# Kernel tuning notes

Hardware: AMD Instinct MI355X
Metric: run time of the kernel (lower is better)

Reference implementation:

```python
import jax, jax.numpy as jnp
import numpy as np

D_HIDDEN = 1024
D_MODEL = 1024
R_MIN, R_MAX = 0.0, 1.0
MAX_PHASE = 6.28
SEQ_LEN = 16384


def setup_inputs() -> dict:
    key = jax.random.key(0)
    k_in, k_th, k_nu, k_bre, k_bim, k_cre, k_cim, k_d = jax.random.split(key, 8)
    inputs = jax.random.normal(k_in, (SEQ_LEN, D_MODEL), dtype=jnp.float32)
    # theta_log ~ log(max_phase * U)
    u_th = jax.random.uniform(k_th, (D_HIDDEN,), dtype=jnp.float32)
    theta_log = jnp.log(MAX_PHASE * u_th)
    # nu_log ~ log(-0.5 * log(U*(r_max^2 - r_min^2) + r_min^2))
    u_nu = jax.random.uniform(k_nu, (D_HIDDEN,), dtype=jnp.float32)
    nu_log = jnp.log(-0.5 * jnp.log(u_nu * (R_MAX**2 - R_MIN**2) + R_MIN**2))
    # gamma_log = log(sqrt(1 - |lambda|^2))
    diag_lambda = jnp.exp(-jnp.exp(nu_log) + 1j * jnp.exp(theta_log))
    gamma_log = jnp.log(jnp.sqrt(1.0 - jnp.abs(diag_lambda) ** 2))
    norm_b = jnp.sqrt(2.0 * D_MODEL)
    norm_c = jnp.sqrt(1.0 * D_HIDDEN)
    B_re = jax.random.normal(k_bre, (D_HIDDEN, D_MODEL), dtype=jnp.float32) / norm_b
    B_im = jax.random.normal(k_bim, (D_HIDDEN, D_MODEL), dtype=jnp.float32) / norm_b
    C_re = jax.random.normal(k_cre, (D_MODEL, D_HIDDEN), dtype=jnp.float32) / norm_c
    C_im = jax.random.normal(k_cim, (D_MODEL, D_HIDDEN), dtype=jnp.float32) / norm_c
    Dp = jax.random.normal(k_d, (D_MODEL,), dtype=jnp.float32)
    return {"inputs": inputs, "nu_log": nu_log, "theta_log": theta_log,
            "gamma_log": gamma_log, "B_re": B_re, "B_im": B_im,
            "C_re": C_re, "C_im": C_im, "Dp": Dp}


def _binop(q_i, q_j):
    # elementwise associative op for diagonal linear recurrence
    A_i, b_i = q_i
    A_j, b_j = q_j
    return (A_j * A_i, A_j * b_i + b_j)


def reference(inputs, nu_log, theta_log, gamma_log, B_re, B_im, C_re, C_im, Dp):
    # diag_lambda: [H] complex64
    diag_lambda = jnp.exp(-jnp.exp(nu_log) + 1j * jnp.exp(theta_log))
    B_norm = (B_re + 1j * B_im) * jnp.exp(gamma_log)[:, None]  # [H, D]
    C = C_re + 1j * C_im                                        # [D, H]
    L = inputs.shape[0]
    # Bu_t = B_norm @ x_t  -> [L, H] complex
    Bu = inputs.astype(B_norm.dtype) @ B_norm.T
    Lambda = jnp.broadcast_to(diag_lambda[None, :], (L, diag_lambda.shape[0]))
    # parallel scan of h_t = lambda * h_{t-1} + Bu_t (initial state = 0)
    _, hidden = jax.lax.associative_scan(_binop, (Lambda, Bu))  # [L, H]
    # y_t = Re[C h_t] + D * x_t
    outputs = jnp.real(hidden @ C.T) + Dp * inputs              # [L, D]
    return (hidden[-1:], outputs)
```

## Files before the change

kernel.cpp:

```cpp
#include <hip/hip_runtime.h>
#include <stdint.h>
#include <stddef.h>

typedef __bf16 bf16;
typedef __attribute__((ext_vector_type(8))) __bf16 bf16x8;
typedef __attribute__((ext_vector_type(4))) __bf16 bf16x4;
typedef __attribute__((ext_vector_type(2))) __bf16 bf16x2;
typedef __attribute__((ext_vector_type(4))) float f32x4;
typedef __attribute__((ext_vector_type(2))) float f32x2;

#define L_SEQ 16384
#define DH    1024
#define DM    1024
#define NH2   2048
#define NC    256
#define LC    (L_SEQ / NC)

__device__ __forceinline__ void async_copy16(const void* g, void* l) {
  __builtin_amdgcn_global_load_lds((const __attribute__((address_space(1))) void*)g,
                                   (__attribute__((address_space(3))) void*)l,
                                   16, 0, 0);
}

__device__ __forceinline__ float bf_lo(uint32_t w) {
  uint32_t u = w << 16; float f; __builtin_memcpy(&f, &u, 4); return f;
}
__device__ __forceinline__ float bf_hi(uint32_t w) {
  uint32_t u = w & 0xffff0000u; float f; __builtin_memcpy(&f, &u, 4); return f;
}

#define NB_CAST 8192
#define NB_W    1024
__global__ void k_prep_all(const float* __restrict__ x, bf16* __restrict__ xb,
                           const float* __restrict__ B_re, const float* __restrict__ B_im,
                           const float* __restrict__ gamma_log, bf16* __restrict__ Wcat,
                           const float* __restrict__ C_re, const float* __restrict__ C_im,
                           bf16* __restrict__ Ccat,
                           const float* __restrict__ nu_log,
                           const float* __restrict__ theta_log,
                           float* __restrict__ lam_re, float* __restrict__ lam_im,
                           float* __restrict__ lamC_re, float* __restrict__ lamC_im) {
  const int b = blockIdx.x;
  if (b < NB_CAST) {
    int i = (b * 256 + (int)threadIdx.x) * 8;
    const float4 a0 = *(const float4*)(x + i);
    const float4 a1 = *(const float4*)(x + i + 4);
    bf16x8 v;
    v[0] = (bf16)a0.x; v[1] = (bf16)a0.y; v[2] = (bf16)a0.z; v[3] = (bf16)a0.w;
    v[4] = (bf16)a1.x; v[5] = (bf16)a1.y; v[6] = (bf16)a1.z; v[7] = (bf16)a1.w;
    *(bf16x8*)(xb + i) = v;
  } else if (b < NB_CAST + NB_W) {
    int idx = ((b - NB_CAST) * 256 + (int)threadIdx.x) * 4;
    int h = idx / DM;
    int d = idx - h * DM;
    float g = expf(gamma_log[h]);
    float4 re = *(const float4*)(B_re + idx);
    float4 im = *(const float4*)(B_im + idx);
    bf16x4 vr, vi;
    vr[0] = (bf16)(re.x * g); vr[1] = (bf16)(re.y * g);
    vr[2] = (bf16)(re.z * g); vr[3] = (bf16)(re.w * g);
    vi[0] = (bf16)(im.x * g); vi[1] = (bf16)(im.y * g);
    vi[2] = (bf16)(im.z * g); vi[3] = (bf16)(im.w * g);
    *(bf16x4*)(Wcat + (size_t)(2 * h) * DM + d)     = vr;
    *(bf16x4*)(Wcat + (size_t)(2 * h + 1) * DM + d) = vi;
  } else if (b < NB_CAST + 2 * NB_W) {
    int idx = ((b - NB_CAST - NB_W) * 256 + (int)threadIdx.x) * 4;
    int d = idx / DH;
    int k = idx - d * DH;
    float4 re = *(const float4*)(C_re + idx);
    float4 im = *(const float4*)(C_im + idx);
    bf16x8 v;
    v[0] = (bf16)re.x; v[1] = (bf16)(-im.x);
    v[2] = (bf16)re.y; v[3] = (bf16)(-im.y);
    v[4] = (bf16)re.z; v[5] = (bf16)(-im.z);
    v[6] = (bf16)re.w; v[7] = (bf16)(-im.w);
    *(bf16x8*)(Ccat + (size_t)d * NH2 + 2 * k) = v;
  } else {
    int h = (b - NB_CAST - 2 * NB_W) * 256 + (int)threadIdx.x;
    if (h < DH) {
      float nu  = expf(nu_log[h]);
      float th  = expf(theta_log[h]);
      float mag = expf(-nu);
      float lr = mag * cosf(th);
      float li = mag * sinf(th);
      lam_re[h] = lr; lam_im[h] = li;
      float ar = lr, ai = li;
#pragma unroll
      for (int i = 0; i < 6; ++i) {
        float nr = ar * ar - ai * ai;
        float ni = 2.f * ar * ai;
        ar = nr; ai = ni;
      }
      lamC_re[h] = ar; lamC_im[h] = ai;
    }
  }
}

template <int MODE>
__global__ __launch_bounds__(256, 3)
void k_gemm(const bf16* __restrict__ A, const bf16* __restrict__ B,
            void* __restrict__ Cout, const float* __restrict__ x,
            const float* __restrict__ dp,
            const float* __restrict__ lam_re, const float* __restrict__ lam_im,
            float* __restrict__ chunk_end, int K, int N) {
  __shared__ char smem[32768];
  bf16* As = (bf16*)smem;
  bf16* Bs = (bf16*)(smem + 16384);
  const int tid  = threadIdx.x;
  const int lane = tid & 63;
  const int wave = tid >> 6;
  const int wm = wave >> 1, wn = wave & 1;
  const int quad = lane >> 4;
  const int l16  = lane & 15;

  const int lin = blockIdx.y * gridDim.x + blockIdx.x;
  const int nY  = gridDim.y;
  const int per = 8 * nY;
  const int sg  = lin / per;
  const int r   = lin - sg * per;
  const int bx  = sg * 8 + (r & 7);
  const int by  = r >> 3;
  const int m0 = bx * 128;
  const int n0 = by * 128;

  f32x4 acc[4][4];
#pragma unroll
  for (int i = 0; i < 4; ++i)
#pragma unroll
    for (int j = 0; j < 4; ++j)
      acc[i][j] = f32x4{0.f, 0.f, 0.f, 0.f};

  for (int k0 = 0; k0 < K; k0 += 64) {
    __syncthreads();
#pragma unroll
    for (int q = 0; q < 4; ++q) {
      const int c = q * 256 + tid;
      const int row = c >> 3, slot = c & 7;
      const int part = slot ^ (row & 7);
      async_copy16(A + (size_t)(m0 + row) * K + k0 + part * 8, (char*)As + c * 16);
      async_copy16(B + (size_t)(n0 + row) * K + k0 + part * 8, (char*)Bs + c * 16);
    }
    __syncthreads();
#pragma unroll
    for (int kk = 0; kk < 64; kk += 32) {
      const int pbase = (kk >> 3);
      bf16x8 fa[4], fb[4];
#pragma unroll
      for (int i = 0; i < 4; ++i) {
        const int ra = wm * 64 + i * 16 + l16;
        const int rb = wn * 64 + i * 16 + l16;
        const int sa = (pbase + quad) ^ (ra & 7);
        const int sb = (pbase + quad) ^ (rb & 7);
        fa[i] = *(const bf16x8*)(As + ra * 64 + sa * 8);
        fb[i] = *(const bf16x8*)(Bs + rb * 64 + sb * 8);
      }
#pragma unroll
      for (int i = 0; i < 4; ++i)
#pragma unroll
        for (int j = 0; j < 4; ++j)
          acc[i][j] = __builtin_amdgcn_mfma_f32_16x16x32_bf16(fa[i], fb[j], acc[i][j], 0, 0, 0);
    }
  }

  if (MODE == 0) {
    __syncthreads();
    bf16* T = (bf16*)smem;
#pragma unroll
    for (int i = 0; i < 4; ++i)
#pragma unroll
      for (int j = 0; j < 4; ++j) {
        const int col = wn * 64 + j * 16 + l16;
        const int grp = col >> 3, cin = col & 7;
#pragma unroll
        for (int p = 0; p < 4; ++p) {
          const int row = wm * 64 + i * 16 + quad * 4 + p;
          T[row * 128 + ((grp ^ (row & 7)) << 3) + cin] = (bf16)acc[i][j][p];
        }
      }
    __syncthreads();
    bf16* out = (bf16*)Cout;
    {
      const int row = tid >> 1, half = tid & 1;
#pragma unroll
      for (int o = 0; o < 8; ++o) {
        const int grp = half * 8 + o;
        bf16x8 v = *(const bf16x8*)(T + row * 128 + ((grp ^ (row & 7)) << 3));
        *(bf16x8*)(out + (size_t)(m0 + row) * N + n0 + grp * 8) = v;
      }
    }
    if (tid < 128) {
      const int ck = tid >> 6;
      const int ch = tid & 63;
      const int gch = (n0 >> 1) + ch;
      const float lr = lam_re[gch], li = lam_im[gch];
      float hr = 0.f, hi = 0.f;
      const int waddr0 = (((ch >> 2) ) << 3) + ((2 * ch) & 7);
#pragma unroll 8
      for (int t = 0; t < 64; ++t) {
        const int row = ck * 64 + t;
        const int grpsw = ((ch >> 2) ^ (row & 7)) << 3;
        uint32_t w = *(const uint32_t*)(T + row * 128 + grpsw + ((2 * ch) & 7));
        float br = bf_lo(w), bi = bf_hi(w);
        float nr = lr * hr - li * hi + br;
        float ni = lr * hi + li * hr + bi;
        hr = nr; hi = ni;
      }
      (void)waddr0;
      *(f32x2*)(chunk_end + (size_t)(2 * bx + ck) * NH2 + n0 + 2 * ch) = f32x2{hr, hi};
    }
  } else {
    float* out = (float*)Cout;
    const int crow0 = m0 + wm * 64 + quad * 4;
    const int ccol0 = n0 + wn * 64 + l16;
#pragma unroll
    for (int j = 0; j < 4; ++j) {
      const int col = ccol0 + j * 16;
      const float dpv = dp[col];
#pragma unroll
      for (int i = 0; i < 4; ++i)
#pragma unroll
        for (int p = 0; p < 4; ++p) {
          const int row = crow0 + i * 16 + p;
          out[(size_t)row * N + col] = acc[i][j][p] + dpv * x[(size_t)row * N + col];
        }
    }
  }
}

__global__ void k_scan_carry(const float* __restrict__ chunk_end,
                             const float* __restrict__ lamC_re,
                             const float* __restrict__ lamC_im,
                             float* __restrict__ carry_in,
                             float* __restrict__ out_final,
                             int interleave) {
  const int h = blockIdx.x * 256 + threadIdx.x;
  const float lr = lamC_re[h], li = lamC_im[h];
  float er = 0.f, ei = 0.f;
#pragma unroll 16
  for (int c = 0; c < NC; ++c) {
    *(f32x2*)(carry_in + (size_t)c * NH2 + 2 * h) = f32x2{er, ei};
    f32x2 ce = *(const f32x2*)(chunk_end + (size_t)c * NH2 + 2 * h);
    float nr = lr * er - li * ei + ce[0];
    float ni = lr * ei + li * er + ce[1];
    er = nr; ei = ni;
  }
  if (interleave) {
    *(f32x2*)(out_final + 2 * h) = f32x2{er, ei};
  } else {
    out_final[h] = er;
  }
}

__global__ void k_scan_apply(bf16* __restrict__ Bu,
                             const float* __restrict__ lam_re,
                             const float* __restrict__ lam_im,
                             const float* __restrict__ carry_in) {
  const int colbase = (blockIdx.y * 256 + (int)threadIdx.x) * 4;
  const int c = blockIdx.x;
  const int h0 = colbase >> 1;
  const float lr0 = lam_re[h0],     li0 = lam_im[h0];
  const float lr1 = lam_re[h0 + 1], li1 = lam_im[h0 + 1];
  f32x4 cv = *(const f32x4*)(carry_in + (size_t)c * NH2 + colbase);
  float hr0 = cv[0], hi0 = cv[1], hr1 = cv[2], hi1 = cv[3];
  bf16* p = Bu + (size_t)c * LC * NH2 + colbase;
#pragma unroll 4
  for (int t = 0; t < LC; ++t) {
    bf16x4 b = *(const bf16x4*)(p);
    float nr0 = lr0 * hr0 - li0 * hi0 + (float)b[0];
    float ni0 = lr0 * hi0 + li0 * hr0 + (float)b[1];
    float nr1 = lr1 * hr1 - li1 * hi1 + (float)b[2];
    float ni1 = lr1 * hi1 + li1 * hr1 + (float)b[3];
    hr0 = nr0; hi0 = ni0; hr1 = nr1; hi1 = ni1;
    bf16x4 wv;
    wv[0] = (bf16)hr0; wv[1] = (bf16)hi0;
    wv[2] = (bf16)hr1; wv[3] = (bf16)hi1;
    *(bf16x4*)(p) = wv;
    p += NH2;
  }
}


extern "C" void kernel_launch(void* const* d_in, const int* in_sizes, int n_in,
                              void* d_out, int out_size, void* d_ws, size_t ws_size,
                              hipStream_t stream) {
  const float* inputs    = (const float*)d_in[0];
  const float* nu_log    = (const float*)d_in[1];
  const float* theta_log = (const float*)d_in[2];
  const float* gamma_log = (const float*)d_in[3];
  const float* B_re      = (const float*)d_in[4];
  const float* B_im      = (const float*)d_in[5];
  const float* C_re      = (const float*)d_in[6];
  const float* C_im      = (const float*)d_in[7];
  const float* Dp        = (const float*)d_in[8];

  char* ws = (char*)d_ws;
  float* lam_re    = (float*)(ws + 0);
  float* lam_im    = (float*)(ws + 4096);
  float* lamC_re   = (float*)(ws + 8192);
  float* lamC_im   = (float*)(ws + 12288);
  float* chunk_end = (float*)(ws + 65536);
  float* carry_in  = (float*)(ws + 65536 + (2u << 20));
  bf16*  Wcat      = (bf16*) (ws + 65536 + (4u << 20));
  bf16*  Ccat      = (bf16*) (ws + 65536 + (8u << 20));
  bf16*  Xb        = (bf16*) (ws + 65536 + (12u << 20));
  bf16*  Bu        = (bf16*) (ws + 65536 + (44u << 20));

  int interleave = 1;
  int state_floats = 2048;
  if (out_size == 1024 + L_SEQ * DM) { interleave = 0; state_floats = 1024; }

  float* out_state = (float*)d_out;
  float* out_y     = (float*)d_out + state_floats;

  k_prep_all<<<dim3(NB_CAST + 2 * NB_W + 4), dim3(256), 0, stream>>>(
      inputs, Xb, B_re, B_im, gamma_log, Wcat, C_re, C_im, Ccat,
      nu_log, theta_log, lam_re, lam_im, lamC_re, lamC_im);

  k_gemm<0><<<dim3(L_SEQ / 128, NH2 / 128), dim3(256), 0, stream>>>(
      Xb, Wcat, (void*)Bu, nullptr, nullptr, lam_re, lam_im, chunk_end, DM, NH2);

  k_scan_carry<<<dim3(4), dim3(256), 0, stream>>>(chunk_end, lamC_re, lamC_im,
                                                  carry_in, out_state, interleave);
  k_scan_apply<<<dim3(NC, 2), dim3(256), 0, stream>>>(Bu, lam_re, lam_im, carry_in);

  k_gemm<1><<<dim3(L_SEQ / 128, DM / 128), dim3(256), 0, stream>>>(
      Bu, Ccat, (void*)out_y, inputs, Dp, nullptr, nullptr, nullptr, NH2, DM);

  (void)in_sizes; (void)n_in; (void)ws_size;
}
```

Baseline: 375.7 us.

## Fuse carry scan into first GEMM via last-block atomic counter

Removes the separate k_scan_carry launch. The last block of the first GEMM to finish, found with an atomic counter plus threadfences, runs the cross-chunk carry scan for all 1024 channels with one 256-thread block. The counter is reset in the prep kernel. Launch bounds are also raised from 3 to 4 waves per SIMD, which may limit registers. The tail scan stays serial on one block, so it trades launch overhead for a serialized tail at the end of the GEMM.

```diff
diff --git a/kernel.cpp b/kernel.cpp
--- a/kernel.cpp
+++ b/kernel.cpp
@@ -39,7 +39,8 @@
                            const float* __restrict__ nu_log,
                            const float* __restrict__ theta_log,
                            float* __restrict__ lam_re, float* __restrict__ lam_im,
-                           float* __restrict__ lamC_re, float* __restrict__ lamC_im) {
+                           float* __restrict__ lamC_re, float* __restrict__ lamC_im,
+                           unsigned int* __restrict__ cnt) {
   const int b = blockIdx.x;
   if (b < NB_CAST) {
     int i = (b * 256 + (int)threadIdx.x) * 8;
@@ -78,6 +79,7 @@
   } else {
     int h = (b - NB_CAST - 2 * NB_W) * 256 + (int)threadIdx.x;
     if (h < DH) {
+      if (h == 0) *cnt = 0u;
       float nu  = expf(nu_log[h]);
       float th  = expf(theta_log[h]);
       float mag = expf(-nu);
@@ -97,12 +99,15 @@
 }
 
 template <int MODE>
-__global__ __launch_bounds__(256, 3)
+__global__ __launch_bounds__(256, 4)
 void k_gemm(const bf16* __restrict__ A, const bf16* __restrict__ B,
             void* __restrict__ Cout, const float* __restrict__ x,
             const float* __restrict__ dp,
             const float* __restrict__ lam_re, const float* __restrict__ lam_im,
-            float* __restrict__ chunk_end, int K, int N) {
+            const float* __restrict__ lamC_re, const float* __restrict__ lamC_im,
+            float* __restrict__ chunk_end, float* __restrict__ carry_in,
+            float* __restrict__ out_state, unsigned int* __restrict__ cnt,
+            int interleave, int K, int N) {
   __shared__ char smem[32768];
   bf16* As = (bf16*)smem;
   bf16* Bs = (bf16*)(smem + 16384);
@@ -194,7 +199,6 @@
       const int gch = (n0 >> 1) + ch;
       const float lr = lam_re[gch], li = lam_im[gch];
       float hr = 0.f, hi = 0.f;
-      const int waddr0 = (((ch >> 2) ) << 3) + ((2 * ch) & 7);
 #pragma unroll 8
       for (int t = 0; t < 64; ++t) {
         const int row = ck * 64 + t;
@@ -205,8 +209,46 @@
         float ni = lr * hi + li * hr + bi;
         hr = nr; hi = ni;
       }
-      (void)waddr0;
       *(f32x2*)(chunk_end + (size_t)(2 * bx + ck) * NH2 + n0 + 2 * ch) = f32x2{hr, hi};
+    }
+
+    __syncthreads();
+    __threadfence();
+    __shared__ int lastFlag;
+    if (tid == 0) {
+      unsigned int old = atomicAdd(cnt, 1u);
+      lastFlag = (old == (unsigned int)(gridDim.x * gridDim.y) - 1u) ? 1 : 0;
+    }
+    __syncthreads();
+    if (lastFlag) {
+      __threadfence();
+      float er[4], ei[4], Lr[4], Li[4];
+#pragma unroll
+      for (int j = 0; j < 4; ++j) {
+        const int h = tid + 256 * j;
+        er[j] = 0.f; ei[j] = 0.f;
+        Lr[j] = lamC_re[h]; Li[j] = lamC_im[h];
+      }
+      for (int c = 0; c < NC; ++c) {
+#pragma unroll
+        for (int j = 0; j < 4; ++j) {
+          const int h = tid + 256 * j;
+          *(f32x2*)(carry_in + (size_t)c * NH2 + 2 * h) = f32x2{er[j], ei[j]};
+          f32x2 ce = *(const f32x2*)(chunk_end + (size_t)c * NH2 + 2 * h);
+          float nr = Lr[j] * er[j] - Li[j] * ei[j] + ce[0];
+          float ni = Lr[j] * ei[j] + Li[j] * er[j] + ce[1];
+          er[j] = nr; ei[j] = ni;
+        }
+      }
+#pragma unroll
+      for (int j = 0; j < 4; ++j) {
+        const int h = tid + 256 * j;
+        if (interleave) {
+          *(f32x2*)(out_state + 2 * h) = f32x2{er[j], ei[j]};
+        } else {
+          out_state[h] = er[j];
+        }
+      }
     }
   } else {
     float* out = (float*)Cout;
@@ -224,30 +266,6 @@
           out[(size_t)row * N + col] = acc[i][j][p] + dpv * x[(size_t)row * N + col];
         }
     }
-  }
-}
-
-__global__ void k_scan_carry(const float* __restrict__ chunk_end,
-                             const float* __restrict__ lamC_re,
-                             const float* __restrict__ lamC_im,
-                             float* __restrict__ carry_in,
-                             float* __restrict__ out_final,
-                             int interleave) {
-  const int h = blockIdx.x * 256 + threadIdx.x;
-  const float lr = lamC_re[h], li = lamC_im[h];
-  float er = 0.f, ei = 0.f;
-#pragma unroll 16
-  for (int c = 0; c < NC; ++c) {
-    *(f32x2*)(carry_in + (size_t)c * NH2 + 2 * h) = f32x2{er, ei};
-    f32x2 ce = *(const f32x2*)(chunk_end + (size_t)c * NH2 + 2 * h);
-    float nr = lr * er - li * ei + ce[0];
-    float ni = lr * ei + li * er + ce[1];
-    er = nr; ei = ni;
-  }
-  if (interleave) {
-    *(f32x2*)(out_final + 2 * h) = f32x2{er, ei};
-  } else {
-    out_final[h] = er;
   }
 }
 
@@ -298,6 +316,7 @@
   float* lam_im    = (float*)(ws + 4096);
   float* lamC_re   = (float*)(ws + 8192);
   float* lamC_im   = (float*)(ws + 12288);
+  unsigned int* cnt = (unsigned int*)(ws + 16384);
   float* chunk_end = (float*)(ws + 65536);
   float* carry_in  = (float*)(ws + 65536 + (2u << 20));
   bf16*  Wcat      = (bf16*) (ws + 65536 + (4u << 20));
@@ -314,17 +333,17 @@
 
   k_prep_all<<<dim3(NB_CAST + 2 * NB_W + 4), dim3(256), 0, stream>>>(
       inputs, Xb, B_re, B_im, gamma_log, Wcat, C_re, C_im, Ccat,
-      nu_log, theta_log, lam_re, lam_im, lamC_re, lamC_im);
+      nu_log, theta_log, lam_re, lam_im, lamC_re, lamC_im, cnt);
 
   k_gemm<0><<<dim3(L_SEQ / 128, NH2 / 128), dim3(256), 0, stream>>>(
-      Xb, Wcat, (void*)Bu, nullptr, nullptr, lam_re, lam_im, chunk_end, DM, NH2);
-
-  k_scan_carry<<<dim3(4), dim3(256), 0, stream>>>(chunk_end, lamC_re, lamC_im,
-                                                  carry_in, out_state, interleave);
+      Xb, Wcat, (void*)Bu, nullptr, nullptr, lam_re, lam_im, lamC_re, lamC_im,
+      chunk_end, carry_in, out_state, cnt, interleave, DM, NH2);
+
   k_scan_apply<<<dim3(NC, 2), dim3(256), 0, stream>>>(Bu, lam_re, lam_im, carry_in);
 
   k_gemm<1><<<dim3(L_SEQ / 128, DM / 128), dim3(256), 0, stream>>>(
-      Bu, Ccat, (void*)out_y, inputs, Dp, nullptr, nullptr, nullptr, NH2, DM);
+      Bu, Ccat, (void*)out_y, inputs, Dp, nullptr, nullptr, nullptr, nullptr,
+      nullptr, nullptr, nullptr, nullptr, 0, NH2, DM);
 
   (void)in_sizes; (void)n_in; (void)ws_size;
 }
```

New measurement: 715.1 us. 90.3% more time.
